# Performance work log

Hardware: AMD Instinct MI355X
Metric: run time of the kernel (lower is better)

## Reference

```python
import jax, jax.numpy as jnp
import numpy as np
from jax import lax

TIME_DIM = 100   # time_feat_dim
MEM_DIM = 172    # node_feat_dim == memory_dim
TAU = 0.3        # energy_threshold
LAM = 0.01       # softshrink sparsity_threshold


def _layer_norm(x, w, b, eps=1e-5):
    m = x.mean(-1, keepdims=True)
    v = ((x - m) ** 2).mean(-1, keepdims=True)
    return (x - m) / jnp.sqrt(v + eps) * w + b


def _time_encode(t):
    # TGN time encoder: cos(t * 1/10^linspace(0,9,D)), fixed (non-trainable)
    freqs = 1.0 / (10.0 ** jnp.linspace(0.0, 9.0, TIME_DIM))
    return jnp.cos(t[..., None] * freqs)


def _softshrink(x, lam=LAM):
    return jnp.where(x > lam, x - lam, jnp.where(x < -lam, x + lam, 0.0))


def setup_inputs() -> dict:
    key = jax.random.key(0)
    ks = jax.random.split(key, 12)
    B, N, NUM_NODES = 8192, 32, 500000
    s = 0.02  # scale used by Global_Local_Filtering
    return {
        "node_ids": jnp.arange(B, dtype=jnp.int32),
        "neighbor_node_ids": jax.random.randint(ks[0], (B, N), 0, NUM_NODES, dtype=jnp.int32),
        "node_interact_times": jax.random.uniform(ks[1], (B,), dtype=jnp.float32) * 1000.0,
        "neighbor_times": jax.random.uniform(ks[2], (B, N), dtype=jnp.float32) * 1000.0,
        "node_memories": jnp.zeros((NUM_NODES, MEM_DIM), jnp.float32),
        "r1": s * jax.random.normal(ks[3], (TIME_DIM, MEM_DIM), jnp.float32),
        "i1": s * jax.random.normal(ks[4], (TIME_DIM, MEM_DIM), jnp.float32),
        "rb1": s * jax.random.normal(ks[5], (MEM_DIM,), jnp.float32),
        "ib1": s * jax.random.normal(ks[6], (MEM_DIM,), jnp.float32),
        "conv_w": 0.02 * jax.random.normal(ks[7], (MEM_DIM, MEM_DIM, 8), jnp.float32),
        "conv_b": 0.02 * jax.random.normal(ks[8], (MEM_DIM,), jnp.float32),
        "rhythm_w": 0.1 * jax.random.normal(ks[9], (272, 1, 4), jnp.float32),
        "lin_w": 0.05 * jax.random.normal(ks[10], (272, MEM_DIM), jnp.float32),
        "lin_b": 0.02 * jax.random.normal(ks[11], (MEM_DIM,), jnp.float32),
        "mb_ln_w": jnp.ones((MEM_DIM,), jnp.float32),
        "mb_ln_b": jnp.zeros((MEM_DIM,), jnp.float32),
        "ln_w": jnp.ones((MEM_DIM,), jnp.float32),
        "ln_b": jnp.zeros((MEM_DIM,), jnp.float32),
    }


def reference(node_ids, neighbor_node_ids, node_interact_times, neighbor_times,
              node_memories, r1, i1, rb1, ib1, conv_w, conv_b,
              rhythm_w, lin_w, lin_b, mb_ln_w, mb_ln_b, ln_w, ln_b):
    # ---- RhythmMemoryUpdater.update_memory ----
    messages = _time_encode(node_interact_times)                 # [B,100]
    old_mem = node_memories[node_ids]                            # [B,172] gather
    x = jnp.concatenate([messages, old_mem], axis=-1)[:, :, None]  # [B,272,1] (NCH)
    # depthwise Conv1d(272,272,k=4,pad=2,groups=272,no bias): length 1 -> 2
    x = lax.conv_general_dilated(x, rhythm_w, (1,), [(2, 2)],
                                 dimension_numbers=("NCH", "OIH", "NCH"),
                                 feature_group_count=272)        # [B,272,2]
    x = jnp.einsum("bcl,cd->bld", x, lin_w) + lin_b              # [B,2,172]
    new_mem = x.mean(axis=1)                                     # mean(dim=1) since 2 != memory_dim
    # set_memories: layer_norm then scatter; then gather + SeqFilter layernorm
    updated = node_memories.at[node_ids].set(_layer_norm(new_mem, mb_ln_w, mb_ln_b))
    gathered = lax.stop_gradient(updated[node_ids])              # memory bank is non-trainable (no_grad)
    root_node_time = _layer_norm(gathered, ln_w, ln_b)           # [B,172]

    # ---- neighbor branch: FSTS (Global_Local_Filtering + Conv1d) ----
    dt = node_interact_times[:, None] - neighbor_times           # [B,N]
    tfeat = _time_encode(dt)                                     # [B,N,100]
    tfeat = jnp.where((neighbor_node_ids == 0)[..., None], 0.0, tfeat)

    xf = jnp.fft.fft(tfeat, axis=1, norm="ortho")                # [B,N,100] complex
    energy = jnp.sum(jnp.abs(xf) ** 2, axis=-1)                  # [B,N]
    mask = (energy / (energy.mean() + 1e-6) >= TAU).astype(tfeat.dtype)
    low = xf * mask[..., None]
    o_r = jnp.einsum("bnc,cd->bnd", low.real, r1) - jnp.einsum("bnc,cd->bnd", low.imag, i1) + rb1
    o_i = jnp.einsum("bnc,cd->bnd", low.imag, r1) + jnp.einsum("bnc,cd->bnd", low.real, i1) + ib1
    y_fft = _softshrink(jax.nn.relu(o_r)) + 1j * _softshrink(jax.nn.relu(o_i))
    y = jnp.fft.ifft(y_fft, axis=1, norm="ortho").real           # [B,N,172]

    # Local_Correlation: Conv1d(172,172,k=8,pad=4) over neighbor axis, then mean over length
    yc = lax.conv_general_dilated(y.transpose(0, 2, 1), conv_w, (1,), [(4, 4)],
                                  dimension_numbers=("NCH", "OIH", "NCH"))
    yc = yc + conv_b[None, :, None]                              # [B,172,33]
    neighbor_out = yc.mean(axis=-1)                              # [B,172]

    return root_node_time + neighbor_out
```

## Files before the change

### kernel.cpp

```cpp
#include <hip/hip_runtime.h>
#include <hip/hip_bf16.h>
#include <math.h>

#define B_ 8192
#define NN 32
#define TD 100
#define MD 172
#define KD 1376
#define TAUC 0.3f
#define LAMC 0.01f

typedef __attribute__((ext_vector_type(8))) short short8;
typedef __attribute__((ext_vector_type(4))) float f32x4;

#define WS_U_OFF    256
#define U_BYTES     ((size_t)B_ * KD * 2)
#define CONVB_ELEMS (11 * 43 * 64 * 8)
#define WBIG_ELEMS  (22 * 7 * 64 * 8)
#define CS_ELEMS    (2 * 64 * 8)
#define ROOT_ELEMS  (11 * 9 * 64 * 8)
#define FRAG_SHORTS (CONVB_ELEMS + WBIG_ELEMS + CS_ELEMS + ROOT_ELEMS)
#define TBL_ELEMS   164

__device__ __forceinline__ float wred(float v) {
#pragma unroll
  for (int o = 32; o > 0; o >>= 1) v += __shfl_down(v, o, 64);
  return v;
}

__device__ __forceinline__ short bf16_bits(float f) {
  __hip_bfloat16 h = __float2bfloat16(f);
  return *(short*)&h;
}

__device__ __forceinline__ unsigned pack2(float a, float b) {
  return (unsigned)(unsigned short)bf16_bits(a) |
         ((unsigned)(unsigned short)bf16_bits(b) << 16);
}

__device__ __forceinline__ float fcos(float x) {
  float r = x * 0.15915494309189535f;
  r = r - floorf(r);
  return __builtin_amdgcn_cosf(r);
}

__global__ __launch_bounds__(256) void k_prep0(
    const float* __restrict__ conv_w, const float* __restrict__ r1,
    const float* __restrict__ i1, const float* __restrict__ rhythm_w,
    const float* __restrict__ lin_w, short* __restrict__ convB,
    short* __restrict__ Wfrag, short* __restrict__ CSfrag,
    short* __restrict__ Rfrag, float* __restrict__ tbl) {
  int idx = blockIdx.x * 256 + threadIdx.x;
  const float inv_s = 0.17677669529663687f;
  if (idx < CONVB_ELEMS) {
    int j = idx & 7;
    int l = (idx >> 3) & 63;
    int s = (idx >> 9) % 43;
    int n0 = idx / (43 * 64 * 8);
    int k = s * 32 + (l >> 4) * 8 + j;
    int col = n0 * 16 + (l & 15);
    float v = (col < MD) ? conv_w[(long)col * KD + k] : 0.f;
    convB[idx] = bf16_bits(v);
    return;
  }
  idx -= CONVB_ELEMS;
  if (idx < WBIG_ELEMS) {
    int j = idx & 7;
    int l = (idx >> 3) & 63;
    int s = (idx % 3584) >> 9;
    int n0 = idx / 3584;
    int k = s * 32 + (l >> 4) * 8 + j;
    int col = n0 * 16 + (l & 15);
    float v = 0.f;
    if (k < 200) {
      if (n0 < 11) {
        int d = col;
        if (d < MD) v = (k < 100) ? r1[k * MD + d] : -i1[(k - 100) * MD + d];
      } else {
        int d = col - 176;
        if (d >= 0 && d < MD) v = (k < 100) ? i1[k * MD + d] : r1[(k - 100) * MD + d];
      }
    }
    Wfrag[idx] = bf16_bits(v);
    return;
  }
  idx -= WBIG_ELEMS;
  if (idx < CS_ELEMS) {
    int j = idx & 7;
    int l = (idx >> 3) & 63;
    int s = idx >> 9;
    int row = l & 15;
    int kq = s * 32 + (l >> 4) * 8 + j;
    float v = 0.f;
    if (row < 8) {
      int kp = (kq < 32) ? kq : kq - 32;
      int lo = row - 4; if (lo < 0) lo = 0;
      int hi = row + 28; if (hi > 31) hi = 31;
      double cs = 0.0, ss = 0.0;
      for (int n = lo; n <= hi; ++n) {
        double ang = 0.19634954084936207740 * (double)((kp * n) & 31);
        cs += cos(ang); ss += sin(ang);
      }
      v = ((kq < 32) ? (float)cs : -(float)ss) * inv_s;
    }
    CSfrag[idx] = bf16_bits(v);
    return;
  }
  idx -= CS_ELEMS;
  if (idx < ROOT_ELEMS) {
    int n = idx / 4608;
    int rem = idx % 4608;
    int s = rem >> 9;
    int l = (rem >> 3) & 63;
    int j = rem & 7;
    int k = s * 32 + (l >> 4) * 8 + j;
    int col = n * 16 + (l & 15);
    float v = 0.f;
    if (k < 272 && col < MD) {
      float hw = 0.5f * (rhythm_w[k * 4 + 1] + rhythm_w[k * 4 + 2]);
      v = hw * lin_w[k * MD + col];
    }
    Rfrag[idx] = bf16_bits(v);
    return;
  }
  idx -= ROOT_ELEMS;
  if (idx < TBL_ELEMS) {
    float v;
    if (idx < 100)      v = (float)exp(-9.0 * (double)idx / 99.0 * 2.302585092994045684);
    else if (idx < 132) v = (float)cos(0.19634954084936207740 * (double)(idx - 100));
    else                v = (float)sin(0.19634954084936207740 * (double)(idx - 132));
    tbl[idx] = v;
  }
}

__global__ __launch_bounds__(256) void k_mean(const int* __restrict__ nid,
                                              const float* __restrict__ t,
                                              const float* __restrict__ nt,
                                              const float* __restrict__ tbl,
                                              float* __restrict__ ws) {
  __shared__ float fr[TD];
  __shared__ float part[4];
  int tid = threadIdx.x;
  if (tid < TD) fr[tid] = tbl[tid];
  __syncthreads();
  int idx = blockIdx.x * 256 + tid;
  int b = idx >> 5;
  float s = 0.f;
  if (nid[idx] != 0) {
    float dt = t[b] - nt[idx];
    for (int c = 0; c < TD; ++c) { float v = fcos(dt * fr[c]); s = fmaf(v, v, s); }
  }
  s = wred(s);
  if ((tid & 63) == 0) part[tid >> 6] = s;
  __syncthreads();
  if (tid == 0) atomicAdd(ws, part[0] + part[1] + part[2] + part[3]);
}

__global__ __launch_bounds__(384, 4) void k_main(
    const int* __restrict__ nbr_id, const float* __restrict__ t,
    const float* __restrict__ nt, const float* __restrict__ rb1,
    const float* __restrict__ ib1, const float* __restrict__ ws0,
    const short* __restrict__ Wfrag, const short* __restrict__ CSfrag,
    const float* __restrict__ tbl, short* __restrict__ u_out) {
  __shared__ __align__(16) short sA[32 * 232];
  __shared__ __align__(16) unsigned char s_un[12800];
  __shared__ float s_fr[TD];
  __shared__ float s_c32[32], s_s32[32], s_dt[32], s_z[32];
  __shared__ float s_energy[32];

  float* tf = (float*)s_un;
  short* Y = (short*)s_un;
  const int tid = threadIdx.x;
  const int b = blockIdx.x;
  const int l = tid & 63, w = tid >> 6;
  const int c = l & 15, q = l >> 4;
  const float inv_s = 0.17677669529663687f;

  if (tid < 32) {
    s_c32[tid] = tbl[100 + tid];
    s_s32[tid] = tbl[132 + tid];
    int gi = b * NN + tid;
    int id = nbr_id[gi];
    float d = t[b] - nt[gi];
    s_z[tid]  = (id == 0) ? 0.f : 1.f;
    s_dt[tid] = (id == 0) ? 0.f : d;
    s_energy[tid] = 0.f;
  }
  if (tid < TD) s_fr[tid] = tbl[tid];
  __syncthreads();

  for (int idx = tid; idx < NN * TD; idx += 384) {
    int n = idx / TD, cc = idx - n * TD;
    tf[idx] = s_z[n] * fcos(s_dt[n] * s_fr[cc]);
  }
  if (tid < 256) {
    int row = tid >> 3, qq = tid & 7;
    *(uint2*)(sA + row * 232 + 200 + qq * 4) = make_uint2(0u, 0u);
  }
  __syncthreads();

  for (int task = tid; task < 17 * 25; task += 384) {
    int k = task / 25, c4 = (task - k * 25) * 4;
    float ar0=0,ar1=0,ar2=0,ar3=0, ai0=0,ai1=0,ai2=0,ai3=0;
    for (int n = 0; n < NN; ++n) {
      float4 a = *(const float4*)(tf + n * TD + c4);
      int j = (k * n) & 31;
      float cw = s_c32[j], sw = s_s32[j];
      ar0 = fmaf(a.x, cw, ar0); ai0 = fmaf(a.x, -sw, ai0);
      ar1 = fmaf(a.y, cw, ar1); ai1 = fmaf(a.y, -sw, ai1);
      ar2 = fmaf(a.z, cw, ar2); ai2 = fmaf(a.z, -sw, ai2);
      ar3 = fmaf(a.w, cw, ar3); ai3 = fmaf(a.w, -sw, ai3);
    }
    ar0*=inv_s; ar1*=inv_s; ar2*=inv_s; ar3*=inv_s;
    ai0*=inv_s; ai1*=inv_s; ai2*=inv_s; ai3*=inv_s;
    float e = ar0*ar0+ar1*ar1+ar2*ar2+ar3*ar3 + ai0*ai0+ai1*ai1+ai2*ai2+ai3*ai3;
    atomicAdd(&s_energy[k], e);
    uint2 vr = make_uint2(pack2(ar0, ar1), pack2(ar2, ar3));
    uint2 vi = make_uint2(pack2(ai0, ai1), pack2(ai2, ai3));
    *(uint2*)(sA + k * 232 + c4) = vr;
    *(uint2*)(sA + k * 232 + 100 + c4) = vi;
    if (k >= 1 && k <= 15) {
      uint2 vin = make_uint2(pack2(-ai0, -ai1), pack2(-ai2, -ai3));
      *(uint2*)(sA + (32 - k) * 232 + c4) = vr;
      *(uint2*)(sA + (32 - k) * 232 + 100 + c4) = vin;
    }
  }
  __syncthreads();

  {
    float gth = TAUC * (ws0[0] * (1.0f / 262144.0f) + 1e-6f);
    for (int idx = tid; idx < 800; idx += 384) {
      int row = idx / 25, qq = idx - row * 25;
      int ks = (row <= 16) ? row : 32 - row;
      if (s_energy[ks] < gth)
        *(uint4*)((char*)sA + row * 464 + qq * 16) = make_uint4(0u,0u,0u,0u);
    }
  }
  __syncthreads();

  short8 A0[7], A1[7];
  {
    const short* a0 = sA + c * 232 + (q << 3);
    const short* a1 = sA + (16 + c) * 232 + (q << 3);
#pragma unroll
    for (int s = 0; s < 7; ++s) {
      A0[s] = *(const short8*)(a0 + s * 32);
      A1[s] = *(const short8*)(a1 + s * 32);
    }
  }

#pragma unroll
  for (int rep = 0; rep < 2; ++rep) {
    int n = w + 6 * rep;
    if (n < 11) {
      f32x4 acc0 = (f32x4)(0.f), acc1 = (f32x4)(0.f);
#pragma unroll
      for (int s = 0; s < 7; ++s) {
        short8 bb = *(const short8*)(Wfrag + (((n * 7 + s) << 6) + l) * 8);
        acc0 = __builtin_amdgcn_mfma_f32_16x16x32_bf16(A0[s], bb, acc0, 0, 0, 0);
        acc1 = __builtin_amdgcn_mfma_f32_16x16x32_bf16(A1[s], bb, acc1, 0, 0, 0);
      }
      int d = n * 16 + c;
      bool valid = (d < MD);
      float bias = valid ? rb1[d] : 0.f;
      f32x4 y0, y1;
#pragma unroll
      for (int r = 0; r < 4; ++r) {
        y0[r] = valid ? fmaxf(acc0[r] + bias - LAMC, 0.f) : 0.f;
        y1[r] = valid ? fmaxf(acc1[r] + bias - LAMC, 0.f) : 0.f;
      }
      *(uint2*)(Y + d * 32 + (q << 2))      = make_uint2(pack2(y0[0], y0[1]), pack2(y0[2], y0[3]));
      *(uint2*)(Y + d * 32 + 16 + (q << 2)) = make_uint2(pack2(y1[0], y1[1]), pack2(y1[2], y1[3]));
    }
  }
  __syncthreads();

  f32x4 uacc[2];
  uacc[0] = (f32x4)(0.f); uacc[1] = (f32x4)(0.f);
  {
    short8 cs0 = *(const short8*)(CSfrag + (l << 3));
#pragma unroll
    for (int ti = 0; ti < 2; ++ti) {
      int nu = w + 6 * ti;
      if (nu < 11) {
        short8 bfr = *(const short8*)(Y + (nu * 16 + c) * 32 + (q << 3));
        uacc[ti] = __builtin_amdgcn_mfma_f32_16x16x32_bf16(cs0, bfr, uacc[ti], 0, 0, 0);
      }
    }
  }
  __syncthreads();

#pragma unroll
  for (int rep = 0; rep < 2; ++rep) {
    int n = w + 6 * rep;
    if (n < 11) {
      int nw = n + 11;
      f32x4 acc0 = (f32x4)(0.f), acc1 = (f32x4)(0.f);
#pragma unroll
      for (int s = 0; s < 7; ++s) {
        short8 bb = *(const short8*)(Wfrag + (((nw * 7 + s) << 6) + l) * 8);
        acc0 = __builtin_amdgcn_mfma_f32_16x16x32_bf16(A0[s], bb, acc0, 0, 0, 0);
        acc1 = __builtin_amdgcn_mfma_f32_16x16x32_bf16(A1[s], bb, acc1, 0, 0, 0);
      }
      int d = n * 16 + c;
      bool valid = (d < MD);
      float bias = valid ? ib1[d] : 0.f;
      f32x4 y0, y1;
#pragma unroll
      for (int r = 0; r < 4; ++r) {
        y0[r] = valid ? fmaxf(acc0[r] + bias - LAMC, 0.f) : 0.f;
        y1[r] = valid ? fmaxf(acc1[r] + bias - LAMC, 0.f) : 0.f;
      }
      *(uint2*)(Y + d * 32 + (q << 2))      = make_uint2(pack2(y0[0], y0[1]), pack2(y0[2], y0[3]));
      *(uint2*)(Y + d * 32 + 16 + (q << 2)) = make_uint2(pack2(y1[0], y1[1]), pack2(y1[2], y1[3]));
    }
  }
  __syncthreads();

  {
    short8 cs1 = *(const short8*)(CSfrag + ((64 + l) << 3));
#pragma unroll
    for (int ti = 0; ti < 2; ++ti) {
      int nu = w + 6 * ti;
      if (nu < 11) {
        short8 bfr = *(const short8*)(Y + (nu * 16 + c) * 32 + (q << 3));
        uacc[ti] = __builtin_amdgcn_mfma_f32_16x16x32_bf16(cs1, bfr, uacc[ti], 0, 0, 0);
        int d = nu * 16 + c;
        if (q < 2 && d < MD) {
          uint2 pv = make_uint2(pack2(uacc[ti][0], uacc[ti][1]),
                                pack2(uacc[ti][2], uacc[ti][3]));
          *(uint2*)(u_out + (long)b * KD + d * 8 + q * 4) = pv;
        }
      }
    }
  }
}

__global__ __launch_bounds__(1024) void k_tail(
    const int* __restrict__ node_ids, const float* __restrict__ t,
    const float* __restrict__ node_mem, const short* __restrict__ u,
    const short* __restrict__ convB, const float* __restrict__ conv_b,
    const short* __restrict__ Rfrag, const float* __restrict__ lin_b,
    const float* __restrict__ mb_w, const float* __restrict__ mb_b,
    const float* __restrict__ ln_w, const float* __restrict__ ln_b,
    const float* __restrict__ tbl, float* __restrict__ out) {
  __shared__ __align__(16) short aR[16 * 296];
  __shared__ __align__(16) float Ct[16 * 176];
  const int tid = threadIdx.x;
  const int l = tid & 63, w = tid >> 6;
  const int c = l & 15, q = l >> 4;
  const int b0 = blockIdx.x * 16;

  for (int idx = tid; idx < 16 * 296; idx += 1024) {
    int r = idx / 296, cc = idx - r * 296;
    float v = 0.f;
    if (cc < TD) v = fcos(t[b0 + r] * tbl[cc]);
    else if (cc < 272) v = node_mem[(long)node_ids[b0 + r] * MD + (cc - TD)];
    aR[idx] = bf16_bits(v);
  }
  __syncthreads();

  f32x4 cacc = (f32x4)(0.f);
  if (w < 11) {
    const short* ap = u + (long)(b0 + c) * KD + (q << 3);
    const short* bp = convB + (((long)w * 43) * 64 + l) * 8;
#pragma unroll 4
    for (int s = 0; s < 43; ++s) {
      short8 a = *(const short8*)(ap + s * 32);
      short8 bb = *(const short8*)(bp + (s << 9));
      cacc = __builtin_amdgcn_mfma_f32_16x16x32_bf16(a, bb, cacc, 0, 0, 0);
    }
  } else {
    const int rstart = (w - 11) * 2;
    const int rcnt = (w == 15) ? 3 : 2;
    f32x4 racc[3];
#pragma unroll
    for (int tt = 0; tt < 3; ++tt) racc[tt] = (f32x4)(0.f);
    const short* arp = aR + c * 296 + (q << 3);
    for (int s = 0; s < 9; ++s) {
      short8 a = *(const short8*)(arp + s * 32);
#pragma unroll
      for (int tt = 0; tt < 3; ++tt) {
        if (tt < rcnt) {
          int n = rstart + tt;
          short8 bb = *(const short8*)(Rfrag + (((n * 9 + s) * 64) + l) * 8);
          racc[tt] = __builtin_amdgcn_mfma_f32_16x16x32_bf16(a, bb, racc[tt], 0, 0, 0);
        }
      }
    }
#pragma unroll
    for (int tt = 0; tt < 3; ++tt) {
      if (tt < rcnt) {
        int n = (rstart + tt) * 16 + c;
#pragma unroll
        for (int r = 0; r < 4; ++r)
          Ct[(q * 4 + r) * 176 + n] = racc[tt][r];
      }
    }
  }
  __syncthreads();

  if (tid < 256) {
    int r = tid >> 4, g = tid & 15;
    float v[11];
    float sm = 0.f, sq = 0.f;
#pragma unroll
    for (int j = 0; j < 11; ++j) {
      int cc = g + 16 * j;
      float x = (cc < MD) ? (Ct[r * 176 + cc] + lin_b[cc]) : 0.f;
      v[j] = x; sm += x; sq += x * x;
    }
#pragma unroll
    for (int m = 1; m < 16; m <<= 1) { sm += __shfl_xor(sm, m, 64); sq += __shfl_xor(sq, m, 64); }
    float mean = sm / 172.f;
    float rstd = rsqrtf(sq / 172.f - mean * mean + 1e-5f);
    float sm2 = 0.f, sq2 = 0.f;
#pragma unroll
    for (int j = 0; j < 11; ++j) {
      int cc = g + 16 * j;
      if (cc < MD) {
        float h = (v[j] - mean) * rstd * mb_w[cc] + mb_b[cc];
        v[j] = h; sm2 += h; sq2 += h * h;
      }
    }
#pragma unroll
    for (int m = 1; m < 16; m <<= 1) { sm2 += __shfl_xor(sm2, m, 64); sq2 += __shfl_xor(sq2, m, 64); }
    float mean2 = sm2 / 172.f;
    float rstd2 = rsqrtf(sq2 / 172.f - mean2 * mean2 + 1e-5f);
#pragma unroll
    for (int j = 0; j < 11; ++j) {
      int cc = g + 16 * j;
      if (cc < MD) Ct[r * 176 + cc] = (v[j] - mean2) * rstd2 * ln_w[cc] + ln_b[cc];
    }
  }
  __syncthreads();

  if (w < 11) {
    int n = w * 16 + c;
    if (n < MD) {
      float cb = conv_b[n];
#pragma unroll
      for (int r = 0; r < 4; ++r) {
        int mr = q * 4 + r;
        out[(long)(b0 + mr) * MD + n] =
            Ct[mr * 176 + n] + cacc[r] * (1.0f / 33.0f) + cb;
      }
    }
  }
}

extern "C" void kernel_launch(void* const* d_in, const int* in_sizes, int n_in,
                              void* d_out, int out_size, void* d_ws, size_t ws_size,
                              hipStream_t stream) {
  const int* node_ids = (const int*)d_in[0];
  const int* nbr_id   = (const int*)d_in[1];
  const float* t  = (const float*)d_in[2];
  const float* nt = (const float*)d_in[3];
  const float* node_mem = (const float*)d_in[4];
  const float* r1 = (const float*)d_in[5];
  const float* i1 = (const float*)d_in[6];
  const float* rb1 = (const float*)d_in[7];
  const float* ib1 = (const float*)d_in[8];
  const float* conv_w = (const float*)d_in[9];
  const float* conv_b = (const float*)d_in[10];
  const float* rhythm_w = (const float*)d_in[11];
  const float* lin_w = (const float*)d_in[12];
  const float* lin_b = (const float*)d_in[13];
  const float* mb_w = (const float*)d_in[14];
  const float* mb_b = (const float*)d_in[15];
  const float* ln_w = (const float*)d_in[16];
  const float* ln_b = (const float*)d_in[17];
  float* out = (float*)d_out;
  float* wsf = (float*)d_ws;

  char* base = (char*)d_ws;
  short* u      = (short*)(base + WS_U_OFF);
  short* convB  = (short*)(base + WS_U_OFF + U_BYTES);
  short* Wfrag  = convB + CONVB_ELEMS;
  short* CSfrag = Wfrag + WBIG_ELEMS;
  short* Rfrag  = CSfrag + CS_ELEMS;
  float* tbl    = (float*)(Rfrag + ROOT_ELEMS);

  hipMemsetAsync(d_ws, 0, 16, stream);
  k_prep0<<<(FRAG_SHORTS + TBL_ELEMS + 255) / 256, 256, 0, stream>>>(
      conv_w, r1, i1, rhythm_w, lin_w, convB, Wfrag, CSfrag, Rfrag, tbl);
  k_mean<<<1024, 256, 0, stream>>>(nbr_id, t, nt, tbl, wsf);
  k_main<<<B_, 384, 0, stream>>>(nbr_id, t, nt, rb1, ib1, wsf, Wfrag, CSfrag, tbl, u);
  k_tail<<<512, 1024, 0, stream>>>(node_ids, t, node_mem, u, convB, conv_b,
                                   Rfrag, lin_b, mb_w, mb_b, ln_w, ln_b, tbl, out);
}
```

Baseline: 634.3 us.

## Compute forward DFT over neighbors with MFMA and split waves across row halves

Replaces the scalar FMA DFT over the 32 neighbor positions with bf16 MFMA against precomputed cos/sin fragment matrices built in the prep kernel. The time features are now written straight to LDS as bf16 in MFMA B-fragment layout. All 32 frequency rows are computed directly instead of mirroring via conjugate symmetry. The later projection GEMMs are reorganised so each wave handles one 16-row half, which halves the A-fragment registers per wave, and launch bounds are raised to target 8 blocks per SM. In exchange, the DFT inputs and twiddles are rounded to bf16 before accumulation, which changes accuracy, and register pressure now has to fit the tighter occupancy target.

```diff
diff --git a/kernel.cpp b/kernel.cpp
--- a/kernel.cpp
+++ b/kernel.cpp
@@ -19,7 +19,8 @@
 #define WBIG_ELEMS  (22 * 7 * 64 * 8)
 #define CS_ELEMS    (2 * 64 * 8)
 #define ROOT_ELEMS  (11 * 9 * 64 * 8)
-#define FRAG_SHORTS (CONVB_ELEMS + WBIG_ELEMS + CS_ELEMS + ROOT_ELEMS)
+#define CS2_ELEMS   (4 * 64 * 8)
+#define FRAG_SHORTS (CONVB_ELEMS + WBIG_ELEMS + CS_ELEMS + ROOT_ELEMS + CS2_ELEMS)
 #define TBL_ELEMS   164
 
 __device__ __forceinline__ float wred(float v) {
@@ -49,7 +50,8 @@
     const float* __restrict__ i1, const float* __restrict__ rhythm_w,
     const float* __restrict__ lin_w, short* __restrict__ convB,
     short* __restrict__ Wfrag, short* __restrict__ CSfrag,
-    short* __restrict__ Rfrag, float* __restrict__ tbl) {
+    short* __restrict__ Rfrag, short* __restrict__ CS2frag,
+    float* __restrict__ tbl) {
   int idx = blockIdx.x * 256 + threadIdx.x;
   const float inv_s = 0.17677669529663687f;
   if (idx < CONVB_ELEMS) {
@@ -124,6 +126,17 @@
     return;
   }
   idx -= ROOT_ELEMS;
+  if (idx < CS2_ELEMS) {
+    int set = idx >> 9, l = (idx >> 3) & 63, j = idx & 7;
+    int mt = set >> 1, isS = set & 1;
+    int kf = mt * 16 + (l & 15);
+    int n = ((l >> 4) << 3) + j;
+    double ang = 0.19634954084936207740 * (double)((kf * n) & 31);
+    double v = isS ? -sin(ang) : cos(ang);
+    CS2frag[idx] = bf16_bits((float)(v * 0.1767766952966368811));
+    return;
+  }
+  idx -= CS2_ELEMS;
   if (idx < TBL_ELEMS) {
     float v;
     if (idx < 100)      v = (float)exp(-9.0 * (double)idx / 99.0 * 2.302585092994045684);
@@ -156,29 +169,27 @@
   if (tid == 0) atomicAdd(ws, part[0] + part[1] + part[2] + part[3]);
 }
 
-__global__ __launch_bounds__(384, 4) void k_main(
+__global__ __launch_bounds__(384, 8) void k_main(
     const int* __restrict__ nbr_id, const float* __restrict__ t,
     const float* __restrict__ nt, const float* __restrict__ rb1,
     const float* __restrict__ ib1, const float* __restrict__ ws0,
     const short* __restrict__ Wfrag, const short* __restrict__ CSfrag,
-    const float* __restrict__ tbl, short* __restrict__ u_out) {
+    const short* __restrict__ CS2frag, const float* __restrict__ tbl,
+    short* __restrict__ u_out) {
   __shared__ __align__(16) short sA[32 * 232];
   __shared__ __align__(16) unsigned char s_un[12800];
   __shared__ float s_fr[TD];
-  __shared__ float s_c32[32], s_s32[32], s_dt[32], s_z[32];
+  __shared__ float s_dt[32], s_z[32];
   __shared__ float s_energy[32];
 
-  float* tf = (float*)s_un;
+  short* sB = (short*)s_un;
   short* Y = (short*)s_un;
   const int tid = threadIdx.x;
   const int b = blockIdx.x;
   const int l = tid & 63, w = tid >> 6;
   const int c = l & 15, q = l >> 4;
-  const float inv_s = 0.17677669529663687f;
 
   if (tid < 32) {
-    s_c32[tid] = tbl[100 + tid];
-    s_s32[tid] = tbl[132 + tid];
     int gi = b * NN + tid;
     int id = nbr_id[gi];
     float d = t[b] - nt[gi];
@@ -189,9 +200,12 @@
   if (tid < TD) s_fr[tid] = tbl[tid];
   __syncthreads();
 
-  for (int idx = tid; idx < NN * TD; idx += 384) {
-    int n = idx / TD, cc = idx - n * TD;
-    tf[idx] = s_z[n] * fcos(s_dt[n] * s_fr[cc]);
+  for (int idx = tid; idx < 3584; idx += 384) {
+    int tt = idx >> 9, ll = (idx >> 3) & 63, j = idx & 7;
+    int n = ((ll >> 4) << 3) + j;
+    int cc = (tt << 4) + (ll & 15);
+    float v = (cc < TD) ? s_z[n] * fcos(s_dt[n] * s_fr[cc]) : 0.f;
+    sB[idx] = bf16_bits(v);
   }
   if (tid < 256) {
     int row = tid >> 3, qq = tid & 7;
@@ -199,30 +213,38 @@
   }
   __syncthreads();
 
-  for (int task = tid; task < 17 * 25; task += 384) {
-    int k = task / 25, c4 = (task - k * 25) * 4;
-    float ar0=0,ar1=0,ar2=0,ar3=0, ai0=0,ai1=0,ai2=0,ai3=0;
-    for (int n = 0; n < NN; ++n) {
-      float4 a = *(const float4*)(tf + n * TD + c4);
-      int j = (k * n) & 31;
-      float cw = s_c32[j], sw = s_s32[j];
-      ar0 = fmaf(a.x, cw, ar0); ai0 = fmaf(a.x, -sw, ai0);
-      ar1 = fmaf(a.y, cw, ar1); ai1 = fmaf(a.y, -sw, ai1);
-      ar2 = fmaf(a.z, cw, ar2); ai2 = fmaf(a.z, -sw, ai2);
-      ar3 = fmaf(a.w, cw, ar3); ai3 = fmaf(a.w, -sw, ai3);
-    }
-    ar0*=inv_s; ar1*=inv_s; ar2*=inv_s; ar3*=inv_s;
-    ai0*=inv_s; ai1*=inv_s; ai2*=inv_s; ai3*=inv_s;
-    float e = ar0*ar0+ar1*ar1+ar2*ar2+ar3*ar3 + ai0*ai0+ai1*ai1+ai2*ai2+ai3*ai3;
-    atomicAdd(&s_energy[k], e);
-    uint2 vr = make_uint2(pack2(ar0, ar1), pack2(ar2, ar3));
-    uint2 vi = make_uint2(pack2(ai0, ai1), pack2(ai2, ai3));
-    *(uint2*)(sA + k * 232 + c4) = vr;
-    *(uint2*)(sA + k * 232 + 100 + c4) = vi;
-    if (k >= 1 && k <= 15) {
-      uint2 vin = make_uint2(pack2(-ai0, -ai1), pack2(-ai2, -ai3));
-      *(uint2*)(sA + (32 - k) * 232 + c4) = vr;
-      *(uint2*)(sA + (32 - k) * 232 + 100 + c4) = vin;
+  const int mside = (w >= 3) ? 1 : 0;
+  const int wn = w % 3;
+  {
+    short8 Ac = *(const short8*)(CS2frag + (((mside << 1) + 0) << 9) + (l << 3));
+    short8 As = *(const short8*)(CS2frag + (((mside << 1) + 1) << 9) + (l << 3));
+    float e4[4] = {0.f, 0.f, 0.f, 0.f};
+    for (int tt = wn; tt < 7; tt += 3) {
+      short8 Bt = *(const short8*)(sB + (tt << 9) + (l << 3));
+      f32x4 xr = (f32x4)(0.f), xi = (f32x4)(0.f);
+      xr = __builtin_amdgcn_mfma_f32_16x16x32_bf16(Ac, Bt, xr, 0, 0, 0);
+      xi = __builtin_amdgcn_mfma_f32_16x16x32_bf16(As, Bt, xi, 0, 0, 0);
+      int cc = (tt << 4) + c;
+      if (cc < TD) {
+#pragma unroll
+        for (int r = 0; r < 4; ++r) {
+          int k = mside * 16 + q * 4 + r;
+          sA[k * 232 + cc]       = bf16_bits(xr[r]);
+          sA[k * 232 + 100 + cc] = bf16_bits(xi[r]);
+          e4[r] = fmaf(xr[r], xr[r], e4[r]);
+          e4[r] = fmaf(xi[r], xi[r], e4[r]);
+        }
+      }
+    }
+#pragma unroll
+    for (int m = 1; m < 16; m <<= 1) {
+#pragma unroll
+      for (int r = 0; r < 4; ++r) e4[r] += __shfl_xor(e4[r], m, 64);
+    }
+    if (c == 0) {
+#pragma unroll
+      for (int r = 0; r < 4; ++r)
+        atomicAdd(&s_energy[mside * 16 + q * 4 + r], e4[r]);
     }
   }
   __syncthreads();
@@ -231,47 +253,35 @@
     float gth = TAUC * (ws0[0] * (1.0f / 262144.0f) + 1e-6f);
     for (int idx = tid; idx < 800; idx += 384) {
       int row = idx / 25, qq = idx - row * 25;
-      int ks = (row <= 16) ? row : 32 - row;
-      if (s_energy[ks] < gth)
+      if (s_energy[row] < gth)
         *(uint4*)((char*)sA + row * 464 + qq * 16) = make_uint4(0u,0u,0u,0u);
     }
   }
   __syncthreads();
 
-  short8 A0[7], A1[7];
+  short8 afrag[7];
   {
-    const short* a0 = sA + c * 232 + (q << 3);
-    const short* a1 = sA + (16 + c) * 232 + (q << 3);
+    const short* ab = sA + (mside * 16 + c) * 232 + (q << 3);
+#pragma unroll
+    for (int s = 0; s < 7; ++s) afrag[s] = *(const short8*)(ab + s * 32);
+  }
+
+  for (int n = wn; n < 11; n += 3) {
+    f32x4 acc = (f32x4)(0.f);
 #pragma unroll
     for (int s = 0; s < 7; ++s) {
-      A0[s] = *(const short8*)(a0 + s * 32);
-      A1[s] = *(const short8*)(a1 + s * 32);
-    }
-  }
-
-#pragma unroll
-  for (int rep = 0; rep < 2; ++rep) {
-    int n = w + 6 * rep;
-    if (n < 11) {
-      f32x4 acc0 = (f32x4)(0.f), acc1 = (f32x4)(0.f);
-#pragma unroll
-      for (int s = 0; s < 7; ++s) {
-        short8 bb = *(const short8*)(Wfrag + (((n * 7 + s) << 6) + l) * 8);
-        acc0 = __builtin_amdgcn_mfma_f32_16x16x32_bf16(A0[s], bb, acc0, 0, 0, 0);
-        acc1 = __builtin_amdgcn_mfma_f32_16x16x32_bf16(A1[s], bb, acc1, 0, 0, 0);
-      }
-      int d = n * 16 + c;
-      bool valid = (d < MD);
-      float bias = valid ? rb1[d] : 0.f;
-      f32x4 y0, y1;
-#pragma unroll
-      for (int r = 0; r < 4; ++r) {
-        y0[r] = valid ? fmaxf(acc0[r] + bias - LAMC, 0.f) : 0.f;
-        y1[r] = valid ? fmaxf(acc1[r] + bias - LAMC, 0.f) : 0.f;
-      }
-      *(uint2*)(Y + d * 32 + (q << 2))      = make_uint2(pack2(y0[0], y0[1]), pack2(y0[2], y0[3]));
-      *(uint2*)(Y + d * 32 + 16 + (q << 2)) = make_uint2(pack2(y1[0], y1[1]), pack2(y1[2], y1[3]));
-    }
+      short8 bb = *(const short8*)(Wfrag + (((n * 7 + s) << 6) + l) * 8);
+      acc = __builtin_amdgcn_mfma_f32_16x16x32_bf16(afrag[s], bb, acc, 0, 0, 0);
+    }
+    int d = n * 16 + c;
+    bool valid = (d < MD);
+    float bias = valid ? rb1[d] : 0.f;
+    float y0 = valid ? fmaxf(acc[0] + bias - LAMC, 0.f) : 0.f;
+    float y1 = valid ? fmaxf(acc[1] + bias - LAMC, 0.f) : 0.f;
+    float y2 = valid ? fmaxf(acc[2] + bias - LAMC, 0.f) : 0.f;
+    float y3 = valid ? fmaxf(acc[3] + bias - LAMC, 0.f) : 0.f;
+    *(uint2*)(Y + d * 32 + mside * 16 + (q << 2)) =
+        make_uint2(pack2(y0, y1), pack2(y2, y3));
   }
   __syncthreads();
 
@@ -290,30 +300,23 @@
   }
   __syncthreads();
 
-#pragma unroll
-  for (int rep = 0; rep < 2; ++rep) {
-    int n = w + 6 * rep;
-    if (n < 11) {
-      int nw = n + 11;
-      f32x4 acc0 = (f32x4)(0.f), acc1 = (f32x4)(0.f);
-#pragma unroll
-      for (int s = 0; s < 7; ++s) {
-        short8 bb = *(const short8*)(Wfrag + (((nw * 7 + s) << 6) + l) * 8);
-        acc0 = __builtin_amdgcn_mfma_f32_16x16x32_bf16(A0[s], bb, acc0, 0, 0, 0);
-        acc1 = __builtin_amdgcn_mfma_f32_16x16x32_bf16(A1[s], bb, acc1, 0, 0, 0);
-      }
-      int d = n * 16 + c;
-      bool valid = (d < MD);
-      float bias = valid ? ib1[d] : 0.f;
-      f32x4 y0, y1;
-#pragma unroll
-      for (int r = 0; r < 4; ++r) {
-        y0[r] = valid ? fmaxf(acc0[r] + bias - LAMC, 0.f) : 0.f;
-        y1[r] = valid ? fmaxf(acc1[r] + bias - LAMC, 0.f) : 0.f;
-      }
-      *(uint2*)(Y + d * 32 + (q << 2))      = make_uint2(pack2(y0[0], y0[1]), pack2(y0[2], y0[3]));
-      *(uint2*)(Y + d * 32 + 16 + (q << 2)) = make_uint2(pack2(y1[0], y1[1]), pack2(y1[2], y1[3]));
-    }
+  for (int n = wn; n < 11; n += 3) {
+    int nw = n + 11;
+    f32x4 acc = (f32x4)(0.f);
+#pragma unroll
+    for (int s = 0; s < 7; ++s) {
+      short8 bb = *(const short8*)(Wfrag + (((nw * 7 + s) << 6) + l) * 8);
+      acc = __builtin_amdgcn_mfma_f32_16x16x32_bf16(afrag[s], bb, acc, 0, 0, 0);
+    }
+    int d = n * 16 + c;
+    bool valid = (d < MD);
+    float bias = valid ? ib1[d] : 0.f;
+    float y0 = valid ? fmaxf(acc[0] + bias - LAMC, 0.f) : 0.f;
+    float y1 = valid ? fmaxf(acc[1] + bias - LAMC, 0.f) : 0.f;
+    float y2 = valid ? fmaxf(acc[2] + bias - LAMC, 0.f) : 0.f;
+    float y3 = valid ? fmaxf(acc[3] + bias - LAMC, 0.f) : 0.f;
+    *(uint2*)(Y + d * 32 + mside * 16 + (q << 2)) =
+        make_uint2(pack2(y0, y1), pack2(y2, y3));
   }
   __syncthreads();
 
@@ -474,18 +477,20 @@
   float* wsf = (float*)d_ws;
 
   char* base = (char*)d_ws;
-  short* u      = (short*)(base + WS_U_OFF);
-  short* convB  = (short*)(base + WS_U_OFF + U_BYTES);
-  short* Wfrag  = convB + CONVB_ELEMS;
-  short* CSfrag = Wfrag + WBIG_ELEMS;
-  short* Rfrag  = CSfrag + CS_ELEMS;
-  float* tbl    = (float*)(Rfrag + ROOT_ELEMS);
+  short* u       = (short*)(base + WS_U_OFF);
+  short* convB   = (short*)(base + WS_U_OFF + U_BYTES);
+  short* Wfrag   = convB + CONVB_ELEMS;
+  short* CSfrag  = Wfrag + WBIG_ELEMS;
+  short* Rfrag   = CSfrag + CS_ELEMS;
+  short* CS2frag = Rfrag + ROOT_ELEMS;
+  float* tbl     = (float*)(CS2frag + CS2_ELEMS);
 
   hipMemsetAsync(d_ws, 0, 16, stream);
   k_prep0<<<(FRAG_SHORTS + TBL_ELEMS + 255) / 256, 256, 0, stream>>>(
-      conv_w, r1, i1, rhythm_w, lin_w, convB, Wfrag, CSfrag, Rfrag, tbl);
+      conv_w, r1, i1, rhythm_w, lin_w, convB, Wfrag, CSfrag, Rfrag, CS2frag, tbl);
   k_mean<<<1024, 256, 0, stream>>>(nbr_id, t, nt, tbl, wsf);
-  k_main<<<B_, 384, 0, stream>>>(nbr_id, t, nt, rb1, ib1, wsf, Wfrag, CSfrag, tbl, u);
+  k_main<<<B_, 384, 0, stream>>>(nbr_id, t, nt, rb1, ib1, wsf,
+                                 Wfrag, CSfrag, CS2frag, tbl, u);
   k_tail<<<512, 1024, 0, stream>>>(node_ids, t, node_mem, u, convB, conv_b,
                                    Rfrag, lin_b, mb_w, mb_b, ln_w, ln_b, tbl, out);
 }
```

Measured after the change: 580.5 us. -8.5%, faster.
